# Optimization experiments

Measured on AMD Instinct MI355X. Metric: run time of the kernel, lower is better.

## Reference

```python
import jax, jax.numpy as jnp
import numpy as np
import math

B, S, DIM = 2, 2048, 1024
H, KVH = 16, 4
HD = DIM // H          # 64, head dim
WINDOW = 256           # sliding-window size (0 = global)
ROPE_BASE = 10000.0
EPS = 1e-6


def setup_inputs() -> dict:
    key = jax.random.key(0)
    ks = jax.random.split(key, 6)
    s = 0.02
    return {
        "x": jax.random.normal(ks[0], (B, S, DIM), jnp.float32),
        "Wq": jax.random.normal(ks[1], (DIM, DIM), jnp.float32) * s,
        "Wk": jax.random.normal(ks[2], (KVH * HD, DIM), jnp.float32) * s,
        "Wv": jax.random.normal(ks[3], (KVH * HD, DIM), jnp.float32) * s,
        "Wo": jax.random.normal(ks[4], (DIM, DIM), jnp.float32) * s,
        "q_gain": jnp.ones((H,), jnp.float32),
        "pair_mix": jnp.tile(jnp.eye(2, dtype=jnp.float32), (H // 2, 1, 1))
                    + 0.01 * jax.random.normal(ks[5], (H // 2, 2, 2), jnp.float32),
    }


def _rms_norm(v):
    # F.rms_norm over last dim, no learned weight
    return v * jax.lax.rsqrt(jnp.mean(v * v, axis=-1, keepdims=True) + EPS)


def _rope_tables(seqlen, dtype):
    inv_freq = 1.0 / (ROPE_BASE ** (jnp.arange(0, HD, 2, dtype=jnp.float32) / HD))  # [HD/2]
    t = jnp.arange(seqlen, dtype=jnp.float32)
    freqs = jnp.outer(t, inv_freq)                        # [S, HD/2]
    return jnp.cos(freqs).astype(dtype)[None, None], jnp.sin(freqs).astype(dtype)[None, None]


def _apply_rotary(v, cos, sin):
    half = v.shape[-1] // 2
    v1, v2 = v[..., :half], v[..., half:]
    return jnp.concatenate((v1 * cos + v2 * sin, -v1 * sin + v2 * cos), axis=-1)


def reference(x, Wq, Wk, Wv, Wo, q_gain, pair_mix):
    bsz, seqlen, dim = x.shape
    q = (x @ Wq.T).reshape(bsz, seqlen, H, HD).transpose(0, 2, 1, 3)    # [B,H,S,D]
    k = (x @ Wk.T).reshape(bsz, seqlen, KVH, HD).transpose(0, 2, 1, 3)  # [B,KV,S,D]
    v = (x @ Wv.T).reshape(bsz, seqlen, KVH, HD).transpose(0, 2, 1, 3)

    q = _rms_norm(q)
    k = _rms_norm(k)
    cos, sin = _rope_tables(seqlen, q.dtype)
    q = _apply_rotary(q, cos, sin)
    k = _apply_rotary(k, cos, sin)
    q = q * q_gain.astype(q.dtype)[None, :, None, None]

    # GQA expansion (repeat_interleave over head axis)
    rep = H // KVH
    k_full = jnp.repeat(k, rep, axis=1)  # [B,H,S,D]
    v_full = jnp.repeat(v, rep, axis=1)

    # sliding-window causal mask: attend iff 0 <= i-j < WINDOW
    pos = jnp.arange(seqlen)
    mask = (pos[:, None] >= pos[None, :]) & (pos[:, None] - pos[None, :] < WINDOW)

    scale = 1.0 / math.sqrt(HD)
    scores = jnp.einsum('bhqd,bhkd->bhqk', q, k_full) * scale
    scores = jnp.where(mask[None, None], scores, jnp.finfo(scores.dtype).min)
    att = jax.nn.softmax(scores, axis=-1)
    y = jnp.einsum('bhqk,bhkd->bhqd', att, v_full)  # [B,H,S,D]

    # paired-head mixing: mix each consecutive head pair with a 2x2 matrix
    yp = y.reshape(bsz, H // 2, 2, seqlen, HD)
    y = jnp.einsum('bpitd,poi->bpotd', yp, pair_mix.astype(y.dtype)).reshape(bsz, H, seqlen, HD)

    out = y.transpose(0, 2, 1, 3).reshape(bsz, seqlen, dim) @ Wo.T
    return out
```

## Files before the change

kernel.cpp:

```cpp
#include <hip/hip_runtime.h>
#include <hip/hip_bf16.h>
#include <cstdint>

#define S_LEN 2048
#define QKV_COLS 1536

typedef __bf16 bf16_t;
typedef bf16_t bf16x8 __attribute__((ext_vector_type(8)));
typedef bf16_t bf16x4 __attribute__((ext_vector_type(4)));
typedef float f32x4 __attribute__((ext_vector_type(4)));

typedef __attribute__((address_space(1))) void as1_void;
typedef __attribute__((address_space(3))) void as3_void;

__device__ __forceinline__ void async_load16(const void* g, void* lds) {
  __builtin_amdgcn_global_load_lds(
      (as1_void*)(uintptr_t)g,
      (as3_void*)(uint32_t)(uintptr_t)lds,
      16, 0, 0);
}

__device__ __forceinline__ uint32_t pkbf(float a, float b) {
  union { bf16_t h[2]; uint32_t u; } c;
  c.h[0] = (bf16_t)a; c.h[1] = (bf16_t)b;
  return c.u;
}

__global__ __launch_bounds__(256) void convert_all(
    const float4* __restrict__ x, const float4* __restrict__ wq,
    const float4* __restrict__ wk, const float4* __restrict__ wv,
    const float4* __restrict__ wo, const float* __restrict__ pm,
    bf16x4* __restrict__ xb, bf16x4* __restrict__ wqkvb, bf16x4* __restrict__ wob) {
  int u = blockIdx.x * 256 + threadIdx.x;
  if (u >= 1441792) {
    int off = u - 1441792;
    int flat = off * 4;
    int row = flat >> 10, colf = flat & 1023;
    int col2p = colf & ~64;
    int p = colf >> 7, ii = (colf >> 6) & 1;
    float4 a = wo[(row * 1024 + col2p) >> 2];
    float4 bq = wo[(row * 1024 + (col2p | 64)) >> 2];
    float m0v = pm[p * 4 + ii], m1v = pm[p * 4 + 2 + ii];
    bf16x4 o4;
    o4[0] = (bf16_t)(m0v * a.x + m1v * bq.x);
    o4[1] = (bf16_t)(m0v * a.y + m1v * bq.y);
    o4[2] = (bf16_t)(m0v * a.z + m1v * bq.z);
    o4[3] = (bf16_t)(m0v * a.w + m1v * bq.w);
    wob[off] = o4;
    return;
  }
  const float4* src; bf16x4* dst; int off;
  if (u < 1048576)      { src = x;  dst = xb;             off = u; }
  else if (u < 1310720) { src = wq; dst = wqkvb;          off = u - 1048576; }
  else if (u < 1376256) { src = wk; dst = wqkvb + 262144; off = u - 1310720; }
  else                  { src = wv; dst = wqkvb + 327680; off = u - 1376256; }
  float4 f = src[off];
  bf16x4 o;
  o[0] = (bf16_t)f.x; o[1] = (bf16_t)f.y; o[2] = (bf16_t)f.z; o[3] = (bf16_t)f.w;
  dst[off] = o;
}

__global__ __launch_bounds__(256) void gemm_qkv(
    const bf16_t* __restrict__ A, const bf16_t* __restrict__ B,
    bf16_t* __restrict__ C, bf16_t* __restrict__ vt,
    const float* __restrict__ q_gain, int N, int K) {
  __shared__ bf16_t As[64 * 64];
  __shared__ bf16_t Bs[128 * 64];
  const int tid = threadIdx.x;
  const int lane = tid & 63;
  const int w = tid >> 6;
  const int wm = (w & 1) << 5, wn = (w >> 1) << 6;
  const int orig = blockIdx.y * gridDim.x + blockIdx.x;
  const int id = (orig & 7) * 96 + (orig >> 3);
  const int m0 = (id / 12) << 6, n0 = (id % 12) << 7;
  const int fidx = lane & 15, quad = lane >> 4;
  f32x4 acc[2][4] = {};
  int ra0 = (tid + 0) >> 3,   sa0 = ((tid + 0) & 7) ^ (ra0 & 7);
  int ra1 = (tid + 256) >> 3, sa1 = ((tid + 256) & 7) ^ (ra1 & 7);
  const bf16_t* Ag0 = A + (size_t)(m0 + ra0) * K + sa0 * 8;
  const bf16_t* Ag1 = A + (size_t)(m0 + ra1) * K + sa1 * 8;
  const bf16_t* Bg[4];
#pragma unroll
  for (int j = 0; j < 4; j++) {
    int c = tid + j * 256, r = c >> 3, s = (c & 7) ^ (r & 7);
    Bg[j] = B + (size_t)(n0 + r) * K + s * 8;
  }
  int aoff[2][2], boff[4][2];
#pragma unroll
  for (int mi = 0; mi < 2; mi++) {
    int row = wm + mi * 16 + fidx;
#pragma unroll
    for (int half = 0; half < 2; half++)
      aoff[mi][half] = row * 64 + (((half * 4 + quad) ^ (row & 7)) * 8);
  }
#pragma unroll
  for (int ni = 0; ni < 4; ni++) {
    int row = wn + ni * 16 + fidx;
#pragma unroll
    for (int half = 0; half < 2; half++)
      boff[ni][half] = row * 64 + (((half * 4 + quad) ^ (row & 7)) * 8);
  }
  for (int kt = 0; kt < K; kt += 64) {
    __syncthreads();
    async_load16(Ag0 + kt, As + tid * 8);
    async_load16(Ag1 + kt, As + (tid + 256) * 8);
#pragma unroll
    for (int j = 0; j < 4; j++)
      async_load16(Bg[j] + kt, Bs + (tid + j * 256) * 8);
    __syncthreads();
    bf16x8 af[2][2], bfr[4][2];
#pragma unroll
    for (int mi = 0; mi < 2; mi++)
#pragma unroll
      for (int half = 0; half < 2; half++)
        af[mi][half] = *(const bf16x8*)(As + aoff[mi][half]);
#pragma unroll
    for (int ni = 0; ni < 4; ni++)
#pragma unroll
      for (int half = 0; half < 2; half++)
        bfr[ni][half] = *(const bf16x8*)(Bs + boff[ni][half]);
#pragma unroll
    for (int half = 0; half < 2; half++)
#pragma unroll
      for (int mi = 0; mi < 2; mi++)
#pragma unroll
        for (int ni = 0; ni < 4; ni++)
          acc[mi][ni] = __builtin_amdgcn_mfma_f32_16x16x32_bf16(
              af[mi][half], bfr[ni][half], acc[mi][ni], 0, 0, 0);
  }
  const int hc0 = n0 + wn;
  if (hc0 >= 1280) {
#pragma unroll
    for (int mi = 0; mi < 2; mi++)
#pragma unroll
      for (int ni = 0; ni < 4; ni++) {
        int cg = (hc0 - 1280) + ni * 16 + fidx;
        int g = cg >> 6, dh = cg & 63;
        int srow = m0 + wm + mi * 16 + quad * 4;
        int bb = srow >> 11, si = srow & (S_LEN - 1);
        bf16x4 pack;
#pragma unroll
        for (int r = 0; r < 4; r++) pack[r] = (bf16_t)acc[mi][ni][r];
        *(bf16x4*)(vt + ((size_t)((bb * 4 + g) * 64 + dh)) * S_LEN + si) = pack;
      }
    return;
  }
  float gain = 1.f;
  if (hc0 < 1024) gain = q_gain[hc0 >> 6] * 0.125f;
#pragma unroll
  for (int mi = 0; mi < 2; mi++)
#pragma unroll
    for (int r = 0; r < 4; r++) {
      float ss = 0.f;
#pragma unroll
      for (int ni = 0; ni < 4; ni++) { float t = acc[mi][ni][r]; ss += t * t; }
#pragma unroll
      for (int off = 8; off >= 1; off >>= 1) ss += __shfl_xor(ss, off);
      float scl = rsqrtf(ss * (1.f / 64.f) + 1e-6f);
      int s = (m0 + wm + mi * 16 + quad * 4 + r) & (S_LEN - 1);
#pragma unroll
      for (int ni = 0; ni < 2; ni++) {
        float v1 = acc[mi][ni][r] * scl;
        float v2 = acc[mi][ni + 2][r] * scl;
        float fr = (float)(ni * 16 + fidx);
        float ang = (float)s * __expf(fr * -0.28782313662425575f);
        float sn, cs;
        __sincosf(ang, &sn, &cs);
        acc[mi][ni][r]     = (v1 * cs + v2 * sn) * gain;
        acc[mi][ni + 2][r] = (-v1 * sn + v2 * cs) * gain;
      }
    }
#pragma unroll
  for (int mi = 0; mi < 2; mi++)
#pragma unroll
    for (int ni = 0; ni < 4; ni++)
#pragma unroll
      for (int r = 0; r < 4; r++) {
        int gr = m0 + wm + mi * 16 + quad * 4 + r;
        int gc = n0 + wn + ni * 16 + fidx;
        C[(size_t)gr * N + gc] = (bf16_t)acc[mi][ni][r];
      }
}

__global__ __launch_bounds__(256) void gemm_bt_f32(
    const bf16_t* __restrict__ A, const bf16_t* __restrict__ B,
    float* __restrict__ C, int N, int K) {
  __shared__ bf16_t As[64 * 64];
  __shared__ bf16_t Bs[128 * 64];
  const int tid = threadIdx.x;
  const int lane = tid & 63;
  const int w = tid >> 6;
  const int wm = (w & 1) << 5, wn = (w >> 1) << 6;
  const int orig = blockIdx.y * gridDim.x + blockIdx.x;
  const int id = (orig & 7) * 64 + (orig >> 3);
  const int m0 = (id >> 3) << 6, n0 = (id & 7) << 7;
  const int fidx = lane & 15, quad = lane >> 4;
  f32x4 acc[2][4] = {};
  int ra0 = (tid + 0) >> 3,   sa0 = ((tid + 0) & 7) ^ (ra0 & 7);
  int ra1 = (tid + 256) >> 3, sa1 = ((tid + 256) & 7) ^ (ra1 & 7);
  const bf16_t* Ag0 = A + (size_t)(m0 + ra0) * K + sa0 * 8;
  const bf16_t* Ag1 = A + (size_t)(m0 + ra1) * K + sa1 * 8;
  const bf16_t* Bg[4];
#pragma unroll
  for (int j = 0; j < 4; j++) {
    int c = tid + j * 256, r = c >> 3, s = (c & 7) ^ (r & 7);
    Bg[j] = B + (size_t)(n0 + r) * K + s * 8;
  }
  int aoff[2][2], boff[4][2];
#pragma unroll
  for (int mi = 0; mi < 2; mi++) {
    int row = wm + mi * 16 + fidx;
#pragma unroll
    for (int half = 0; half < 2; half++)
      aoff[mi][half] = row * 64 + (((half * 4 + quad) ^ (row & 7)) * 8);
  }
#pragma unroll
  for (int ni = 0; ni < 4; ni++) {
    int row = wn + ni * 16 + fidx;
#pragma unroll
    for (int half = 0; half < 2; half++)
      boff[ni][half] = row * 64 + (((half * 4 + quad) ^ (row & 7)) * 8);
  }
  for (int kt = 0; kt < K; kt += 64) {
    __syncthreads();
    async_load16(Ag0 + kt, As + tid * 8);
    async_load16(Ag1 + kt, As + (tid + 256) * 8);
#pragma unroll
    for (int j = 0; j < 4; j++)
      async_load16(Bg[j] + kt, Bs + (tid + j * 256) * 8);
    __syncthreads();
    bf16x8 af[2][2], bfr[4][2];
#pragma unroll
    for (int mi = 0; mi < 2; mi++)
#pragma unroll
      for (int half = 0; half < 2; half++)
        af[mi][half] = *(const bf16x8*)(As + aoff[mi][half]);
#pragma unroll
    for (int ni = 0; ni < 4; ni++)
#pragma unroll
      for (int half = 0; half < 2; half++)
        bfr[ni][half] = *(const bf16x8*)(Bs + boff[ni][half]);
#pragma unroll
    for (int half = 0; half < 2; half++)
#pragma unroll
      for (int mi = 0; mi < 2; mi++)
#pragma unroll
        for (int ni = 0; ni < 4; ni++)
          acc[mi][ni] = __builtin_amdgcn_mfma_f32_16x16x32_bf16(
              af[mi][half], bfr[ni][half], acc[mi][ni], 0, 0, 0);
  }
#pragma unroll
  for (int mi = 0; mi < 2; mi++)
#pragma unroll
    for (int ni = 0; ni < 4; ni++)
#pragma unroll
      for (int r = 0; r < 4; r++) {
        int gr = m0 + wm + mi * 16 + quad * 4 + r;
        int gc = n0 + wn + ni * 16 + fidx;
        C[(size_t)gr * N + gc] = acc[mi][ni][r];
      }
}

#define FIXMAX 8.0f
#define OST 72
__global__ __launch_bounds__(256) void attn_mfma(
    const bf16_t* __restrict__ qkv, const bf16_t* __restrict__ vt,
    bf16_t* __restrict__ yb) {
  __shared__ bf16_t ob[4][32 * OST];
  const int tid = threadIdx.x, lane = tid & 63, w = tid >> 6;
  const int col = lane & 15, quad = lane >> 4;
  const int orig = blockIdx.z * 256 + blockIdx.y * 64 + blockIdx.x;
  const int id = (orig & 7) * 64 + (orig >> 3);
  const int q0 = (id & 63) * 32, g = (id >> 6) & 3, b = id >> 8;
  const int h = g * 4 + w;

  bf16x8 qf[2][2];
#pragma unroll
  for (int t = 0; t < 2; t++) {
    const bf16_t* qb =
        qkv + ((size_t)b * S_LEN + q0 + t * 16 + col) * QKV_COLS + h * 64 + quad * 8;
    qf[t][0] = *(const bf16x8*)qb;
    qf[t][1] = *(const bf16x8*)(qb + 32);
  }
  const bf16_t* kbase = qkv + (size_t)b * S_LEN * QKV_COLS + 1024 + g * 64 + quad * 8;
  const bf16_t* vbase = vt + ((size_t)((b * 4 + g) * 64) + col) * S_LEN + quad * 8;

  f32x4 o[2][4] = {};
  float ps[2] = {};

  const int c_lo = max(0, (q0 - 255) >> 5);
  const int c_hi = (q0 + 31) >> 5;
  for (int c = c_lo; c <= c_hi; c++) {
    const int k0 = c * 32;
    bf16x8 kf[2][2];
#pragma unroll
    for (int nt = 0; nt < 2; nt++) {
      const bf16_t* kp = kbase + (size_t)(k0 + nt * 16 + col) * QKV_COLS;
      kf[nt][0] = *(const bf16x8*)kp;
      kf[nt][1] = *(const bf16x8*)(kp + 32);
    }
    bf16x8 vf[4];
#pragma unroll
    for (int nt2 = 0; nt2 < 4; nt2++)
      vf[nt2] = *(const bf16x8*)(vbase + (size_t)(nt2 * 16) * S_LEN + k0);

#pragma unroll
    for (int t = 0; t < 2; t++) {
      const int qt0 = q0 + t * 16;
      if (k0 > qt0 + 15) continue;
      f32x4 st[2];
#pragma unroll
      for (int nt = 0; nt < 2; nt++) {
        f32x4 a = {};
        a = __builtin_amdgcn_mfma_f32_16x16x32_bf16(kf[nt][0], qf[t][0], a, 0, 0, 0);
        a = __builtin_amdgcn_mfma_f32_16x16x32_bf16(kf[nt][1], qf[t][1], a, 0, 0, 0);
        st[nt] = a;
      }
      const bool needmask = (k0 + 31 > qt0) || (k0 < qt0 - 224);
      float p2[2][4];
      if (needmask) {
        int q = qt0 + col;
#pragma unroll
        for (int nt = 0; nt < 2; nt++)
#pragma unroll
          for (int r = 0; r < 4; r++) {
            int k = k0 + nt * 16 + quad * 4 + r;
            bool valid = (k <= q) && (q - k < 256);
            p2[nt][r] = valid ? __expf(st[nt][r] - FIXMAX) : 0.f;
          }
      } else {
#pragma unroll
        for (int nt = 0; nt < 2; nt++)
#pragma unroll
          for (int r = 0; r < 4; r++)
            p2[nt][r] = __expf(st[nt][r] - FIXMAX);
      }
#pragma unroll
      for (int nt = 0; nt < 2; nt++)
#pragma unroll
        for (int r = 0; r < 4; r++) ps[t] += p2[nt][r];
      uint32_t pk0[2], pk1[2];
      pk0[0] = pkbf(p2[0][0], p2[0][1]); pk0[1] = pkbf(p2[0][2], p2[0][3]);
      pk1[0] = pkbf(p2[1][0], p2[1][1]); pk1[1] = pkbf(p2[1][2], p2[1][3]);
      uint32_t w32[4];
#pragma unroll
      for (int m = 0; m < 4; m++) {
        int srclane = col + 16 * ((2 * quad + (m >> 1)) & 3);
        uint32_t a0 = (uint32_t)__shfl((int)pk0[m & 1], srclane);
        uint32_t a1 = (uint32_t)__shfl((int)pk1[m & 1], srclane);
        w32[m] = (quad < 2) ? a0 : a1;
      }
      union { uint32_t u[4]; bf16x8 v; } pu;
      pu.u[0] = w32[0]; pu.u[1] = w32[1]; pu.u[2] = w32[2]; pu.u[3] = w32[3];
      bf16x8 pf = pu.v;
#pragma unroll
      for (int nt2 = 0; nt2 < 4; nt2++)
        o[t][nt2] = __builtin_amdgcn_mfma_f32_16x16x32_bf16(pf, vf[nt2], o[t][nt2], 0, 0, 0);
    }
  }
#pragma unroll
  for (int t = 0; t < 2; t++) {
    float v = ps[t];
    v += __shfl_xor(v, 16);
    v += __shfl_xor(v, 32);
    float il = 1.f / v;
    float il4[4];
#pragma unroll
    for (int r = 0; r < 4; r++) il4[r] = __shfl(il, quad * 4 + r);
    int row0 = t * 16 + quad * 4;
#pragma unroll
    for (int nt2 = 0; nt2 < 4; nt2++)
#pragma unroll
      for (int r = 0; r < 4; r++)
        ob[w][(row0 + r) * OST + nt2 * 16 + col] = (bf16_t)(o[t][nt2][r] * il4[r]);
  }
  asm volatile("s_waitcnt lgkmcnt(0)" ::: "memory");
#pragma unroll
  for (int it = 0; it < 4; it++) {
    int row = it * 8 + (lane >> 3);
    int d0 = (lane & 7) * 8;
    bf16x8 v8 = *(const bf16x8*)(ob[w] + row * OST + d0);
    *(bf16x8*)(yb + ((size_t)b * S_LEN + q0 + row) * 1024 + h * 64 + d0) = v8;
  }
}

extern "C" void kernel_launch(void* const* d_in, const int* in_sizes, int n_in,
                              void* d_out, int out_size, void* d_ws, size_t ws_size,
                              hipStream_t stream) {
  const float* x        = (const float*)d_in[0];
  const float* Wq       = (const float*)d_in[1];
  const float* Wk       = (const float*)d_in[2];
  const float* Wv       = (const float*)d_in[3];
  const float* Wo       = (const float*)d_in[4];
  const float* q_gain   = (const float*)d_in[5];
  const float* pair_mix = (const float*)d_in[6];
  float* out = (float*)d_out;

  bf16_t* ws    = (bf16_t*)d_ws;
  bf16_t* xb    = ws;
  bf16_t* wqkvb = xb + 4096 * 1024;
  bf16_t* wob   = wqkvb + 1536 * 1024;
  bf16_t* qkvb  = wob + 1024 * 1024;
  bf16_t* yb    = qkvb + 4096 * 1536;
  bf16_t* vt    = yb + 4096 * 1024;

  convert_all<<<6656, 256, 0, stream>>>(
      (const float4*)x, (const float4*)Wq, (const float4*)Wk, (const float4*)Wv,
      (const float4*)Wo, pair_mix, (bf16x4*)xb, (bf16x4*)wqkvb, (bf16x4*)wob);
  gemm_qkv<<<dim3(12, 64), 256, 0, stream>>>(xb, wqkvb, qkvb, vt, q_gain, 1536, 1024);
  attn_mfma<<<dim3(64, 4, 2), 256, 0, stream>>>(qkvb, vt, yb);
  gemm_bt_f32<<<dim3(8, 64), 256, 0, stream>>>(yb, wob, out, 1024, 1024);
}
```

Before: 142.2 us.

## Double-buffer LDS tiles in QKV and output GEMMs to overlap loads

Both GEMM kernels now keep two LDS buffers for the A and B tiles. The next K-tile is prefetched with async global-to-LDS loads while the current tile feeds the MFMAs, and partial vmcnt waits plus explicit barriers replace the two __syncthreads per iteration. This aims to hide global load latency behind compute. In exchange LDS use doubles to 48KB per block, which may reduce occupancy, and correctness now relies on the hand-written waitcnt counts.

```diff
diff --git a/kernel.cpp b/kernel.cpp
--- a/kernel.cpp
+++ b/kernel.cpp
@@ -64,8 +64,8 @@
     const bf16_t* __restrict__ A, const bf16_t* __restrict__ B,
     bf16_t* __restrict__ C, bf16_t* __restrict__ vt,
     const float* __restrict__ q_gain, int N, int K) {
-  __shared__ bf16_t As[64 * 64];
-  __shared__ bf16_t Bs[128 * 64];
+  __shared__ bf16_t As[2][64 * 64];
+  __shared__ bf16_t Bs[2][128 * 64];
   const int tid = threadIdx.x;
   const int lane = tid & 63;
   const int w = tid >> 6;
@@ -100,25 +100,37 @@
     for (int half = 0; half < 2; half++)
       boff[ni][half] = row * 64 + (((half * 4 + quad) ^ (row & 7)) * 8);
   }
+  async_load16(Ag0, &As[0][tid * 8]);
+  async_load16(Ag1, &As[0][(tid + 256) * 8]);
+#pragma unroll
+  for (int j = 0; j < 4; j++)
+    async_load16(Bg[j], &Bs[0][(tid + j * 256) * 8]);
+  int cur = 0;
   for (int kt = 0; kt < K; kt += 64) {
-    __syncthreads();
-    async_load16(Ag0 + kt, As + tid * 8);
-    async_load16(Ag1 + kt, As + (tid + 256) * 8);
-#pragma unroll
-    for (int j = 0; j < 4; j++)
-      async_load16(Bg[j] + kt, Bs + (tid + j * 256) * 8);
-    __syncthreads();
+    const int nk = kt + 64;
+    if (nk < K) {
+      async_load16(Ag0 + nk, &As[cur ^ 1][tid * 8]);
+      async_load16(Ag1 + nk, &As[cur ^ 1][(tid + 256) * 8]);
+#pragma unroll
+      for (int j = 0; j < 4; j++)
+        async_load16(Bg[j] + nk, &Bs[cur ^ 1][(tid + j * 256) * 8]);
+      asm volatile("s_waitcnt vmcnt(6)" ::: "memory");
+    } else {
+      asm volatile("s_waitcnt vmcnt(0)" ::: "memory");
+    }
+    __builtin_amdgcn_s_barrier();
+    __builtin_amdgcn_sched_barrier(0);
     bf16x8 af[2][2], bfr[4][2];
 #pragma unroll
     for (int mi = 0; mi < 2; mi++)
 #pragma unroll
       for (int half = 0; half < 2; half++)
-        af[mi][half] = *(const bf16x8*)(As + aoff[mi][half]);
+        af[mi][half] = *(const bf16x8*)(&As[cur][aoff[mi][half]]);
 #pragma unroll
     for (int ni = 0; ni < 4; ni++)
 #pragma unroll
       for (int half = 0; half < 2; half++)
-        bfr[ni][half] = *(const bf16x8*)(Bs + boff[ni][half]);
+        bfr[ni][half] = *(const bf16x8*)(&Bs[cur][boff[ni][half]]);
 #pragma unroll
     for (int half = 0; half < 2; half++)
 #pragma unroll
@@ -127,6 +139,9 @@
         for (int ni = 0; ni < 4; ni++)
           acc[mi][ni] = __builtin_amdgcn_mfma_f32_16x16x32_bf16(
               af[mi][half], bfr[ni][half], acc[mi][ni], 0, 0, 0);
+    asm volatile("s_waitcnt lgkmcnt(0)" ::: "memory");
+    __builtin_amdgcn_s_barrier();
+    cur ^= 1;
   }
   const int hc0 = n0 + wn;
   if (hc0 >= 1280) {
@@ -185,8 +200,8 @@
 __global__ __launch_bounds__(256) void gemm_bt_f32(
     const bf16_t* __restrict__ A, const bf16_t* __restrict__ B,
     float* __restrict__ C, int N, int K) {
-  __shared__ bf16_t As[64 * 64];
-  __shared__ bf16_t Bs[128 * 64];
+  __shared__ bf16_t As[2][64 * 64];
+  __shared__ bf16_t Bs[2][128 * 64];
   const int tid = threadIdx.x;
   const int lane = tid & 63;
   const int w = tid >> 6;
@@ -221,25 +236,37 @@
     for (int half = 0; half < 2; half++)
       boff[ni][half] = row * 64 + (((half * 4 + quad) ^ (row & 7)) * 8);
   }
+  async_load16(Ag0, &As[0][tid * 8]);
+  async_load16(Ag1, &As[0][(tid + 256) * 8]);
+#pragma unroll
+  for (int j = 0; j < 4; j++)
+    async_load16(Bg[j], &Bs[0][(tid + j * 256) * 8]);
+  int cur = 0;
   for (int kt = 0; kt < K; kt += 64) {
-    __syncthreads();
-    async_load16(Ag0 + kt, As + tid * 8);
-    async_load16(Ag1 + kt, As + (tid + 256) * 8);
-#pragma unroll
-    for (int j = 0; j < 4; j++)
-      async_load16(Bg[j] + kt, Bs + (tid + j * 256) * 8);
-    __syncthreads();
+    const int nk = kt + 64;
+    if (nk < K) {
+      async_load16(Ag0 + nk, &As[cur ^ 1][tid * 8]);
+      async_load16(Ag1 + nk, &As[cur ^ 1][(tid + 256) * 8]);
+#pragma unroll
+      for (int j = 0; j < 4; j++)
+        async_load16(Bg[j] + nk, &Bs[cur ^ 1][(tid + j * 256) * 8]);
+      asm volatile("s_waitcnt vmcnt(6)" ::: "memory");
+    } else {
+      asm volatile("s_waitcnt vmcnt(0)" ::: "memory");
+    }
+    __builtin_amdgcn_s_barrier();
+    __builtin_amdgcn_sched_barrier(0);
     bf16x8 af[2][2], bfr[4][2];
 #pragma unroll
     for (int mi = 0; mi < 2; mi++)
 #pragma unroll
       for (int half = 0; half < 2; half++)
-        af[mi][half] = *(const bf16x8*)(As + aoff[mi][half]);
+        af[mi][half] = *(const bf16x8*)(&As[cur][aoff[mi][half]]);
 #pragma unroll
     for (int ni = 0; ni < 4; ni++)
 #pragma unroll
       for (int half = 0; half < 2; half++)
-        bfr[ni][half] = *(const bf16x8*)(Bs + boff[ni][half]);
+        bfr[ni][half] = *(const bf16x8*)(&Bs[cur][boff[ni][half]]);
 #pragma unroll
     for (int half = 0; half < 2; half++)
 #pragma unroll
@@ -248,6 +275,9 @@
         for (int ni = 0; ni < 4; ni++)
           acc[mi][ni] = __builtin_amdgcn_mfma_f32_16x16x32_bf16(
               af[mi][half], bfr[ni][half], acc[mi][ni], 0, 0, 0);
+    asm volatile("s_waitcnt lgkmcnt(0)" ::: "memory");
+    __builtin_amdgcn_s_barrier();
+    cur ^= 1;
   }
 #pragma unroll
   for (int mi = 0; mi < 2; mi++)
```

Result: faster. 137.6 us (-3.3%).
